# Optimization experiments

Hardware: AMD Instinct MI355X
Metric: run time of the kernel (lower is better)

Reference implementation:

```python
import jax, jax.numpy as jnp
import numpy as np

RADIUS = 0.8
NSAMPLE = 32
EPS = 1e-5  # BatchNorm eps


def _bn(x, gamma, beta, axes):
    # BatchNorm (training-mode batch statistics), channel dim kept via broadcasting
    m = jnp.mean(x, axis=axes, keepdims=True)
    v = jnp.var(x, axis=axes, keepdims=True)
    return (x - m) * jax.lax.rsqrt(v + EPS) * gamma + beta


def setup_inputs() -> dict:
    key = jax.random.key(0)
    ks = jax.random.split(key, 6)
    B, N, P, C, COUT = 4, 8192, 2048, 128, 256
    ffps_xyz = jax.random.uniform(ks[0], (B, P, 3), dtype=jnp.float32) * 2.0 - 1.0
    backbone_xyz = jax.random.uniform(ks[1], (B, N, 3), dtype=jnp.float32) * 2.0 - 1.0
    backbone_features = jax.random.normal(ks[2], (B, C, N), dtype=jnp.float32)
    w_shift = jax.random.normal(ks[3], (3, 3), dtype=jnp.float32) * 0.1
    gamma_shift = jnp.ones((3,), jnp.float32)
    beta_shift = jnp.zeros((3,), jnp.float32)
    w_mlp = jax.random.normal(ks[4], (COUT, 3 + C), dtype=jnp.float32) * 0.05
    gamma_mlp = jnp.ones((COUT,), jnp.float32)
    beta_mlp = jnp.zeros((COUT,), jnp.float32)
    return {
        "ffps_xyz": ffps_xyz,
        "backbone_xyz": backbone_xyz,
        "backbone_features": backbone_features,
        "w_shift": w_shift,
        "gamma_shift": gamma_shift,
        "beta_shift": beta_shift,
        "w_mlp": w_mlp,
        "gamma_mlp": gamma_mlp,
        "beta_mlp": beta_mlp,
    }


def reference(ffps_xyz, backbone_xyz, backbone_features,
              w_shift, gamma_shift, beta_shift,
              w_mlp, gamma_mlp, beta_mlp):
    B, P, _ = ffps_xyz.shape
    N = backbone_xyz.shape[1]

    # ---- shift_layer: Conv1d(3->3, k=1, no bias) + BN1d + ReLU on (B,3,P) ----
    x = jnp.einsum('oc,bpc->bop', w_shift, ffps_xyz)                  # (B,3,P)
    x = _bn(x, gamma_shift[None, :, None], beta_shift[None, :, None], (0, 2))
    new_xyz = jax.nn.relu(x).transpose(0, 2, 1)                       # (B,P,3) query centers

    # ---- QueryAndGroup: ball query (radius, nsample), use_xyz=True ----
    d2 = jnp.sum((new_xyz[:, :, None, :] - backbone_xyz[:, None, :, :]) ** 2, -1)  # (B,P,N)
    within = d2 < (RADIUS * RADIUS)
    # pick the first NSAMPLE in-radius indices (CUDA ball_query semantics)
    keyv = jnp.where(within, jnp.arange(N, dtype=jnp.int32), jnp.int32(N))
    negk, idx = jax.lax.top_k(-keyv, NSAMPLE)                          # smallest keys first
    valid = (-negk) < N
    idx = jnp.where(valid, idx, idx[..., :1])                          # pad with first found idx

    g_xyz = jnp.take_along_axis(backbone_xyz[:, None, :, :], idx[..., None], axis=2)
    g_xyz = g_xyz - new_xyz[:, :, None, :]                             # (B,P,S,3) recentered
    feats = backbone_features.transpose(0, 2, 1)                       # (B,N,C)
    g_f = jnp.take_along_axis(feats[:, None, :, :], idx[..., None], axis=2)  # (B,P,S,C)
    g = jnp.concatenate([g_xyz, g_f], axis=-1)                         # (B,P,S,3+C)

    # ---- mlp: 1x1 conv (3+C -> COUT, no bias) + BN + ReLU ----
    y = jnp.einsum('oc,bpsc->bops', w_mlp, g)                          # (B,COUT,P,S)
    y = _bn(y, gamma_mlp[None, :, None, None], beta_mlp[None, :, None, None], (0, 2, 3))
    y = jax.nn.relu(y)

    # ---- max-pool over neighbor axis, squeeze, transpose ----
    y = jnp.max(y, axis=3)                                             # (B,COUT,P)
    return y.transpose(0, 2, 1)                                        # (B,P,COUT)
```

## Files before the change

kernel.cpp:

```cpp
#include <hip/hip_runtime.h>
#include <math.h>

namespace {
constexpr int B    = 4;
constexpr int N    = 8192;
constexpr int P    = 2048;
constexpr int C    = 128;
constexpr int COUT = 256;
constexpr int NS   = 32;
constexpr int BP   = B * P;
constexpr int BPB  = 2;
constexpr int GRP  = 8;
constexpr int NBLK = BP / (BPB * GRP);

constexpr size_t OFF_FEATT = 0;
constexpr size_t OFF_WSWZ  = 8388608;
constexpr size_t OFF_NXD   = 8470528;
constexpr size_t OFF_NXF   = 8667136;
constexpr size_t OFF_IDX   = 8765440;
constexpr size_t OFF_YMAX  = 9814016;
constexpr size_t OFF_PART  = 18202624;
constexpr size_t OFF_P2    = 19251200;
constexpr size_t OFF_AB    = 19513344;
constexpr size_t WS_NEED   = 19515392;
}

typedef short bf16x8 __attribute__((ext_vector_type(8)));
typedef float f32x4  __attribute__((ext_vector_type(4)));

typedef const __attribute__((address_space(1))) void gas_void;
typedef __attribute__((address_space(3))) void las_void;
#define GLOBAL_LOAD_LDS16(gp, lp) \
    __builtin_amdgcn_global_load_lds((gas_void*)(gp), (las_void*)(lp), 16, 0, 0)

__device__ inline unsigned short f2bf(float f) {
    unsigned u = __float_as_uint(f);
    unsigned r = u + 0x7fffu + ((u >> 16) & 1u);
    return (unsigned short)(r >> 16);
}

__global__ __launch_bounds__(256) void k_transpose(const float* __restrict__ feat,
                                                   unsigned short* __restrict__ featT) {
    __shared__ float tile[64][33];
    int tx = threadIdx.x, ty = threadIdx.y;
    int n0 = blockIdx.x * 32, c0 = blockIdx.y * 64, b = blockIdx.z;
    const float* src = feat + ((size_t)b * C + c0) * N + n0;
#pragma unroll
    for (int j = 0; j < 8; j++) tile[ty + 8 * j][tx] = src[(size_t)(ty + 8 * j) * N + tx];
    __syncthreads();
    int t = ty * 32 + tx;
    int n = t >> 3;
    int k8 = (t & 7) * 8;
    unsigned vv[4];
#pragma unroll
    for (int i = 0; i < 4; i++) {
        unsigned lo = f2bf(tile[k8 + 2 * i][n]);
        unsigned hi = f2bf(tile[k8 + 2 * i + 1][n]);
        vv[i] = lo | (hi << 16);
    }
    *(int4*)&featT[((size_t)b * N + n0 + n) * C + c0 + k8] =
        make_int4((int)vv[0], (int)vv[1], (int)vv[2], (int)vv[3]);
}

__global__ __launch_bounds__(256) void k_wswz(const float* __restrict__ w,
                                              unsigned short* __restrict__ wswz) {
    int i = blockIdx.x * 256 + threadIdx.x;
    int j = i & 7;
    int lane = (i >> 3) & 63;
    int rest = i >> 9;
    int ks = rest % 5, rt = rest / 5;
    int cout = rt * 16 + (lane & 15);
    int k = ks * 32 + (lane >> 4) * 8 + j;
    float v = 0.f;
    if (k < 128) v = w[cout * 131 + 3 + k];
    else if (k < 131) v = w[cout * 131 + (k - 128)];
    wswz[i] = f2bf(v);
}

__global__ __launch_bounds__(1024) void k_shift(const float* __restrict__ ffps,
                                                const float* __restrict__ wsh,
                                                const float* __restrict__ gam,
                                                const float* __restrict__ bet,
                                                double* __restrict__ nxd,
                                                float* __restrict__ nxf) {
#pragma clang fp contract(off)
    __shared__ double red[6][1024];
    __shared__ double par[6];
    int t = threadIdx.x;
    double w[9];
#pragma unroll
    for (int i = 0; i < 9; i++) w[i] = (double)wsh[i];
    double x[8][3];
    double s[3] = {0, 0, 0}, sq[3] = {0, 0, 0};
#pragma unroll
    for (int i = 0; i < 8; i++) {
        int p = t + 1024 * i;
        double f0 = (double)ffps[p * 3 + 0];
        double f1 = (double)ffps[p * 3 + 1];
        double f2 = (double)ffps[p * 3 + 2];
#pragma unroll
        for (int o = 0; o < 3; o++) {
            double xo = (w[o * 3 + 0] * f0 + w[o * 3 + 1] * f1) + w[o * 3 + 2] * f2;
            x[i][o] = xo;
            s[o] += xo;
            sq[o] += xo * xo;
        }
    }
#pragma unroll
    for (int o = 0; o < 3; o++) { red[o][t] = s[o]; red[3 + o][t] = sq[o]; }
    for (int off = 512; off > 0; off >>= 1) {
        __syncthreads();
        if (t < off) {
#pragma unroll
            for (int j = 0; j < 6; j++) red[j][t] += red[j][t + off];
        }
    }
    __syncthreads();
    if (t == 0) {
#pragma unroll
        for (int o = 0; o < 3; o++) {
            double m = red[o][0] / (double)BP;
            double v = red[3 + o][0] / (double)BP - m * m;
            par[o] = m;
            par[3 + o] = 1.0 / sqrt(v + 1e-5);
        }
    }
    __syncthreads();
    double gv[3] = {(double)gam[0], (double)gam[1], (double)gam[2]};
    double bv[3] = {(double)bet[0], (double)bet[1], (double)bet[2]};
#pragma unroll
    for (int i = 0; i < 8; i++) {
        int p = t + 1024 * i;
#pragma unroll
        for (int o = 0; o < 3; o++) {
            double y = ((x[i][o] - par[o]) * par[3 + o]) * gv[o] + bv[o];
            y = (y > 0.0) ? y : 0.0;
            nxd[p * 3 + o] = y;
            nxf[p * 3 + o] = (float)y;
        }
    }
}

__global__ __launch_bounds__(256) void k_ballq(const float* __restrict__ bbxyz,
                                               const double* __restrict__ nxd,
                                               int* __restrict__ idxo) {
#pragma clang fp contract(off)
    int t = threadIdx.x;
    int wv = t >> 6, lane = t & 63;
    int q = blockIdx.x * 4 + wv;
    int b = q >> 11;
    double qx = nxd[q * 3 + 0], qy = nxd[q * 3 + 1], qz = nxd[q * 3 + 2];
    const double R2 = 0.8 * 0.8;
    {
        double ex = fmax(fmax(qx - 1.0, -1.0 - qx), 0.0);
        double ey = fmax(fmax(qy - 1.0, -1.0 - qy), 0.0);
        double ez = fmax(fmax(qz - 1.0, -1.0 - qz), 0.0);
        if (ex * ex + ey * ey + ez * ez >= R2) {
            if (lane < NS) idxo[q * NS + lane] = 0;
            return;
        }
    }
    const float* base = bbxyz + (size_t)b * N * 3;
    int found = 0, firstn = -1;

    float X0[8], Y0[8], Z0[8], X1[8], Y1[8], Z1[8], X2[8], Y2[8], Z2[8];

    auto loadb = [&](float (&XX)[8], float (&YY)[8], float (&ZZ)[8], int it) {
#pragma unroll
        for (int j = 0; j < 8; j++) {
            int n = it * 512 + j * 64 + lane;
            XX[j] = base[n * 3 + 0];
            YY[j] = base[n * 3 + 1];
            ZZ[j] = base[n * 3 + 2];
        }
    };
    auto proc = [&](float (&XX)[8], float (&YY)[8], float (&ZZ)[8], int it) {
#pragma clang fp contract(off)
#pragma unroll
        for (int j = 0; j < 8; j++) {
            int n = it * 512 + j * 64 + lane;
            double dx = qx - (double)XX[j];
            double dy = qy - (double)YY[j];
            double dz = qz - (double)ZZ[j];
            double d2 = (dx * dx + dy * dy) + dz * dz;
            bool within = d2 < R2;
            unsigned long long mask = __ballot(within);
            if (firstn < 0 && mask != 0ull) firstn = (n - lane) + (__ffsll(mask) - 1);
            if (within) {
                int rank = found + __popcll(mask & ((1ull << lane) - 1ull));
                if (rank < NS) idxo[q * NS + rank] = n;
            }
            found += __popcll(mask);
        }
    };

    loadb(X0, Y0, Z0, 0);
    loadb(X1, Y1, Z1, 1);
    loadb(X2, Y2, Z2, 2);

    for (int itb = 0; itb < 16; itb += 3) {
        proc(X0, Y0, Z0, itb);
        if (found >= NS) break;
        loadb(X0, Y0, Z0, (itb + 3 < 16) ? itb + 3 : 0);
        if (itb + 1 >= 16) break;
        proc(X1, Y1, Z1, itb + 1);
        if (found >= NS) break;
        loadb(X1, Y1, Z1, (itb + 4 < 16) ? itb + 4 : 0);
        if (itb + 2 >= 16) break;
        proc(X2, Y2, Z2, itb + 2);
        if (found >= NS) break;
        loadb(X2, Y2, Z2, (itb + 5 < 16) ? itb + 5 : 0);
    }
    if (found < NS) {
        int padv = (found == 0) ? 0 : firstn;
        if (lane >= found && lane < NS) idxo[q * NS + lane] = padv;
    }
}

__global__ __launch_bounds__(256, 2) void k_mlp_mfma(
        const float* __restrict__ bbxyz,
        const unsigned short* __restrict__ featT,
        const unsigned short* __restrict__ wswz,
        const float* __restrict__ nxf,
        const int* __restrict__ idx,
        float* __restrict__ ymax,
        float* __restrict__ partial) {
    __shared__ alignas(16) unsigned short G[2][4 * 4 * 64 * 8];
    int t = threadIdx.x, lane = t & 63, w = t >> 6;
    int q = lane >> 4, c16 = lane & 15;
    int blk = blockIdx.x;
    int bpbase = blk * (BPB * GRP);
    const bf16x8* wp = (const bf16x8*)wswz;

    bf16x8 wreg[5][4];
#pragma unroll
    for (int ks = 0; ks < 5; ks++)
#pragma unroll
        for (int nt = 0; nt < 4; nt++)
            wreg[ks][nt] = wp[((w * 4 + nt) * 5 + ks) * 64 + lane];

    int n_cur[4], n_nxt[4], n_nx2[4];
#pragma unroll
    for (int mt = 0; mt < 4; mt++)
        n_cur[mt] = idx[(bpbase + (mt >> 1)) * NS + (mt & 1) * 16 + c16];
#pragma unroll
    for (int mt = 0; mt < 4; mt++)
        n_nxt[mt] = idx[(bpbase + BPB + (mt >> 1)) * NS + (mt & 1) * 16 + c16];
    {
        int bp = bpbase + (w >> 1);
        const unsigned short* row = featT + ((size_t)(bp >> 11) * N + n_cur[w]) * C + q * 8;
#pragma unroll
        for (int ks = 0; ks < 4; ks++)
            GLOBAL_LOAD_LDS16(row + ks * 32, &G[0][(w * 4 + ks) * 512]);
    }

    float smA[4] = {0.f, 0.f, 0.f, 0.f}, sqA[4] = {0.f, 0.f, 0.f, 0.f};

    for (int g = 0; g < GRP; g++) {
        int buf = g & 1;
        int bp0 = bpbase + g * BPB;
        if (g + 2 < GRP) {
#pragma unroll
            for (int mt = 0; mt < 4; mt++)
                n_nx2[mt] = idx[(bp0 + 2 * BPB + (mt >> 1)) * NS + (mt & 1) * 16 + c16];
        }
        __syncthreads();
        if (g + 1 < GRP) {
            int bp = bp0 + BPB + (w >> 1);
            const unsigned short* row = featT + ((size_t)(bp >> 11) * N + n_nxt[w]) * C + q * 8;
#pragma unroll
            for (int ks = 0; ks < 4; ks++)
                GLOBAL_LOAD_LDS16(row + ks * 32, &G[buf ^ 1][(w * 4 + ks) * 512]);
        }

        f32x4 acc[4][4];
#pragma unroll
        for (int mt = 0; mt < 4; mt++)
#pragma unroll
            for (int nt = 0; nt < 4; nt++) acc[mt][nt] = (f32x4){0.f, 0.f, 0.f, 0.f};

#pragma unroll
        for (int ks = 0; ks < 4; ks++) {
            bf16x8 ag[4];
#pragma unroll
            for (int mt = 0; mt < 4; mt++)
                ag[mt] = *(const bf16x8*)&G[buf][((mt * 4 + ks) * 64 + lane) * 8];
#pragma unroll
            for (int nt = 0; nt < 4; nt++)
#pragma unroll
                for (int mt = 0; mt < 4; mt++)
                    acc[mt][nt] = __builtin_amdgcn_mfma_f32_16x16x32_bf16(ag[mt], wreg[ks][nt], acc[mt][nt], 0, 0, 0);
        }
        {
            bf16x8 agx[4];
#pragma unroll
            for (int mt = 0; mt < 4; mt++) {
                int bp = bp0 + (mt >> 1);
                unsigned u01 = 0, u23 = 0;
                if (q == 0) {
                    const float* src = bbxyz + ((size_t)(bp >> 11) * N + n_cur[mt]) * 3;
                    const float* ctr = nxf + bp * 3;
                    u01 = (unsigned)f2bf(src[0] - ctr[0]) | ((unsigned)f2bf(src[1] - ctr[1]) << 16);
                    u23 = (unsigned)f2bf(src[2] - ctr[2]);
                }
                union { int4 i; bf16x8 h; } u;
                u.i = make_int4((int)u01, (int)u23, 0, 0);
                agx[mt] = u.h;
            }
#pragma unroll
            for (int nt = 0; nt < 4; nt++)
#pragma unroll
                for (int mt = 0; mt < 4; mt++)
                    acc[mt][nt] = __builtin_amdgcn_mfma_f32_16x16x32_bf16(agx[mt], wreg[4][nt], acc[mt][nt], 0, 0, 0);
        }

#pragma unroll
        for (int pm = 0; pm < BPB; pm++) {
            int bp = bp0 + pm;
#pragma unroll
            for (int nt = 0; nt < 4; nt++) {
                f32x4 a = acc[2 * pm][nt], c = acc[2 * pm + 1][nt];
                float mx = fmaxf(fmaxf(fmaxf(a[0], a[1]), fmaxf(a[2], a[3])),
                                 fmaxf(fmaxf(c[0], c[1]), fmaxf(c[2], c[3])));
                smA[nt] += ((a[0] + a[1]) + (a[2] + a[3])) + ((c[0] + c[1]) + (c[2] + c[3]));
                sqA[nt] += ((a[0] * a[0] + a[1] * a[1]) + (a[2] * a[2] + a[3] * a[3])) +
                           ((c[0] * c[0] + c[1] * c[1]) + (c[2] * c[2] + c[3] * c[3]));
                mx = fmaxf(mx, __shfl_xor(mx, 16, 64));
                mx = fmaxf(mx, __shfl_xor(mx, 32, 64));
                if (q == 0)
                    ymax[(size_t)bp * COUT + w * 64 + nt * 16 + c16] = mx;
            }
        }
#pragma unroll
        for (int mt = 0; mt < 4; mt++) { n_cur[mt] = n_nxt[mt]; n_nxt[mt] = n_nx2[mt]; }
    }

#pragma unroll
    for (int nt = 0; nt < 4; nt++) {
        float sm = smA[nt], sq = sqA[nt];
        sm += __shfl_xor(sm, 16, 64);
        sm += __shfl_xor(sm, 32, 64);
        sq += __shfl_xor(sq, 16, 64);
        sq += __shfl_xor(sq, 32, 64);
        if (q == 0) {
            int cout = w * 64 + nt * 16 + c16;
            partial[(size_t)blk * 512 + cout] = sm;
            partial[(size_t)blk * 512 + 256 + cout] = sq;
        }
    }
}

__global__ __launch_bounds__(256) void k_red(const float* __restrict__ partial,
                                             float* __restrict__ p2) {
    int t = threadIdx.x, j = blockIdx.x;
    const float* row = partial + (size_t)j * 4 * 512;
    float s0 = 0.f, s1 = 0.f;
    for (int r = 0; r < 4; r++) {
        s0 += row[r * 512 + t];
        s1 += row[r * 512 + 256 + t];
    }
    p2[j * 512 + t] = s0;
    p2[j * 512 + 256 + t] = s1;
}

__global__ __launch_bounds__(256) void k_stats(const float* __restrict__ p2,
                                               const float* __restrict__ gam,
                                               const float* __restrict__ bet,
                                               float* __restrict__ ab) {
    int c = threadIdx.x;
    double sm = 0.0, sq = 0.0;
    for (int r = 0; r < 128; r++) {
        sm += (double)p2[r * 512 + c];
        sq += (double)p2[r * 512 + 256 + c];
    }
    const double cnt = (double)BP * (double)NS;
    double mean = sm / cnt;
    double var = sq / cnt - mean * mean;
    double a = (double)gam[c] / sqrt(var + 1e-5);
    double bb = (double)bet[c] - mean * a;
    ab[c] = (float)a;
    ab[256 + c] = (float)bb;
}

__global__ __launch_bounds__(256) void k_final(const float* __restrict__ ymax,
                                               const float* __restrict__ ab,
                                               float* __restrict__ out) {
    int i = blockIdx.x * 256 + threadIdx.x;
    int c0 = (i & 63) * 4;
    f32x4 y = *(const f32x4*)&ymax[(size_t)i * 4];
    f32x4 a = *(const f32x4*)&ab[c0];
    f32x4 bb = *(const f32x4*)&ab[256 + c0];
    f32x4 r;
#pragma unroll
    for (int j = 0; j < 4; j++) r[j] = fmaxf(a[j] * y[j] + bb[j], 0.f);
    *(f32x4*)&out[(size_t)i * 4] = r;
}

extern "C" void kernel_launch(void* const* d_in, const int* in_sizes, int n_in,
                              void* d_out, int out_size, void* d_ws, size_t ws_size,
                              hipStream_t stream) {
    const float* ffps  = (const float*)d_in[0];
    const float* bbxyz = (const float*)d_in[1];
    const float* feat  = (const float*)d_in[2];
    const float* wsh   = (const float*)d_in[3];
    const float* gsh   = (const float*)d_in[4];
    const float* bsh   = (const float*)d_in[5];
    const float* wml   = (const float*)d_in[6];
    const float* gml   = (const float*)d_in[7];
    const float* bml   = (const float*)d_in[8];
    float* out = (float*)d_out;
    char* ws = (char*)d_ws;
    if (ws_size < WS_NEED) return;

    unsigned short* featT = (unsigned short*)(ws + OFF_FEATT);
    unsigned short* wswz  = (unsigned short*)(ws + OFF_WSWZ);
    double*         nxd   = (double*)(ws + OFF_NXD);
    float*          nxf   = (float*)(ws + OFF_NXF);
    int*            idx   = (int*)(ws + OFF_IDX);
    float*          ymax  = (float*)(ws + OFF_YMAX);
    float*          part  = (float*)(ws + OFF_PART);
    float*          p2    = (float*)(ws + OFF_P2);
    float*          ab    = (float*)(ws + OFF_AB);

    k_transpose<<<dim3(N / 32, C / 64, B), dim3(32, 8, 1), 0, stream>>>(feat, featT);
    k_wswz<<<dim3(160), dim3(256), 0, stream>>>(wml, wswz);
    k_shift<<<dim3(1), dim3(1024), 0, stream>>>(ffps, wsh, gsh, bsh, nxd, nxf);
    k_ballq<<<dim3(BP / 4), dim3(256), 0, stream>>>(bbxyz, nxd, idx);
    k_mlp_mfma<<<dim3(NBLK), dim3(256), 0, stream>>>(bbxyz, featT, wswz, nxf, idx, ymax, part);
    k_red<<<dim3(128), dim3(256), 0, stream>>>(part, p2);
    k_stats<<<dim3(1), dim3(256), 0, stream>>>(p2, gml, bml, ab);
    k_final<<<dim3(BP * COUT / 1024), dim3(256), 0, stream>>>(ymax, ab, out);
}
```

Measured before the change: 169.9 us.

## Fuse front-end kernels and replace partial-sum reduction with atomics

Eight launches are collapsed into four. A multi-block prep kernel produces the shift-layer partial statistics, and one combined front kernel runs the feature transpose, weight swizzle, shift normalisation and ball query. The MLP kernel now accumulates the BN statistics with float atomics into zeroed sums, and the final kernel computes the scale and shift inline, so the separate reduction and stats kernels go away. This removes launch gaps and the serial single-block kernels, but float atomic accumulation makes the summation order nondeterministic, and every final block recomputes the per-channel statistics.

```diff
diff --git a/kernel.cpp b/kernel.cpp
--- a/kernel.cpp
+++ b/kernel.cpp
@@ -15,14 +15,12 @@
 
 constexpr size_t OFF_FEATT = 0;
 constexpr size_t OFF_WSWZ  = 8388608;
-constexpr size_t OFF_NXD   = 8470528;
-constexpr size_t OFF_NXF   = 8667136;
-constexpr size_t OFF_IDX   = 8765440;
-constexpr size_t OFF_YMAX  = 9814016;
-constexpr size_t OFF_PART  = 18202624;
-constexpr size_t OFF_P2    = 19251200;
-constexpr size_t OFF_AB    = 19513344;
-constexpr size_t WS_NEED   = 19515392;
+constexpr size_t OFF_SSLOT = 8470528;
+constexpr size_t OFF_SUMS  = 8471040;
+constexpr size_t OFF_NXF   = 8475136;
+constexpr size_t OFF_IDX   = 8573440;
+constexpr size_t OFF_YMAX  = 9622016;
+constexpr size_t WS_NEED   = 18010624;
 }
 
 typedef short bf16x8 __attribute__((ext_vector_type(8)));
@@ -39,76 +37,37 @@
     return (unsigned short)(r >> 16);
 }
 
-__global__ __launch_bounds__(256) void k_transpose(const float* __restrict__ feat,
-                                                   unsigned short* __restrict__ featT) {
-    __shared__ float tile[64][33];
-    int tx = threadIdx.x, ty = threadIdx.y;
-    int n0 = blockIdx.x * 32, c0 = blockIdx.y * 64, b = blockIdx.z;
-    const float* src = feat + ((size_t)b * C + c0) * N + n0;
-#pragma unroll
-    for (int j = 0; j < 8; j++) tile[ty + 8 * j][tx] = src[(size_t)(ty + 8 * j) * N + tx];
-    __syncthreads();
-    int t = ty * 32 + tx;
-    int n = t >> 3;
-    int k8 = (t & 7) * 8;
-    unsigned vv[4];
+__global__ __launch_bounds__(256) void k_prep(const float* __restrict__ ffps,
+                                              const float* __restrict__ wsh,
+                                              double* __restrict__ sslot,
+                                              float* __restrict__ sums) {
+#pragma clang fp contract(off)
+    int blk = blockIdx.x, t = threadIdx.x;
+    if (blk == 8) {
+        ((f32x4*)sums)[t & 127] = (f32x4){0.f, 0.f, 0.f, 0.f};
+        return;
+    }
+    __shared__ double red[6][256];
+    double w[9];
+#pragma unroll
+    for (int i = 0; i < 9; i++) w[i] = (double)wsh[i];
+    double s[3] = {0, 0, 0}, sq[3] = {0, 0, 0};
 #pragma unroll
     for (int i = 0; i < 4; i++) {
-        unsigned lo = f2bf(tile[k8 + 2 * i][n]);
-        unsigned hi = f2bf(tile[k8 + 2 * i + 1][n]);
-        vv[i] = lo | (hi << 16);
-    }
-    *(int4*)&featT[((size_t)b * N + n0 + n) * C + c0 + k8] =
-        make_int4((int)vv[0], (int)vv[1], (int)vv[2], (int)vv[3]);
-}
-
-__global__ __launch_bounds__(256) void k_wswz(const float* __restrict__ w,
-                                              unsigned short* __restrict__ wswz) {
-    int i = blockIdx.x * 256 + threadIdx.x;
-    int j = i & 7;
-    int lane = (i >> 3) & 63;
-    int rest = i >> 9;
-    int ks = rest % 5, rt = rest / 5;
-    int cout = rt * 16 + (lane & 15);
-    int k = ks * 32 + (lane >> 4) * 8 + j;
-    float v = 0.f;
-    if (k < 128) v = w[cout * 131 + 3 + k];
-    else if (k < 131) v = w[cout * 131 + (k - 128)];
-    wswz[i] = f2bf(v);
-}
-
-__global__ __launch_bounds__(1024) void k_shift(const float* __restrict__ ffps,
-                                                const float* __restrict__ wsh,
-                                                const float* __restrict__ gam,
-                                                const float* __restrict__ bet,
-                                                double* __restrict__ nxd,
-                                                float* __restrict__ nxf) {
-#pragma clang fp contract(off)
-    __shared__ double red[6][1024];
-    __shared__ double par[6];
-    int t = threadIdx.x;
-    double w[9];
-#pragma unroll
-    for (int i = 0; i < 9; i++) w[i] = (double)wsh[i];
-    double x[8][3];
-    double s[3] = {0, 0, 0}, sq[3] = {0, 0, 0};
-#pragma unroll
-    for (int i = 0; i < 8; i++) {
-        int p = t + 1024 * i;
+        int p = blk * 1024 + t + 256 * i;
         double f0 = (double)ffps[p * 3 + 0];
         double f1 = (double)ffps[p * 3 + 1];
         double f2 = (double)ffps[p * 3 + 2];
 #pragma unroll
         for (int o = 0; o < 3; o++) {
             double xo = (w[o * 3 + 0] * f0 + w[o * 3 + 1] * f1) + w[o * 3 + 2] * f2;
-            x[i][o] = xo;
             s[o] += xo;
             sq[o] += xo * xo;
         }
     }
 #pragma unroll
     for (int o = 0; o < 3; o++) { red[o][t] = s[o]; red[3 + o][t] = sq[o]; }
-    for (int off = 512; off > 0; off >>= 1) {
+    for (int off = 128; off > 0; off >>= 1) {
         __syncthreads();
         if (t < off) {
 #pragma unroll
@@ -116,40 +75,90 @@
         }
     }
     __syncthreads();
-    if (t == 0) {
-#pragma unroll
-        for (int o = 0; o < 3; o++) {
-            double m = red[o][0] / (double)BP;
-            double v = red[3 + o][0] / (double)BP - m * m;
-            par[o] = m;
-            par[3 + o] = 1.0 / sqrt(v + 1e-5);
-        }
-    }
-    __syncthreads();
-    double gv[3] = {(double)gam[0], (double)gam[1], (double)gam[2]};
-    double bv[3] = {(double)bet[0], (double)bet[1], (double)bet[2]};
-#pragma unroll
-    for (int i = 0; i < 8; i++) {
-        int p = t + 1024 * i;
-#pragma unroll
-        for (int o = 0; o < 3; o++) {
-            double y = ((x[i][o] - par[o]) * par[3 + o]) * gv[o] + bv[o];
-            y = (y > 0.0) ? y : 0.0;
-            nxd[p * 3 + o] = y;
-            nxf[p * 3 + o] = (float)y;
-        }
-    }
-}
-
-__global__ __launch_bounds__(256) void k_ballq(const float* __restrict__ bbxyz,
-                                               const double* __restrict__ nxd,
+    if (t < 6) sslot[blk * 6 + t] = red[t][0];
+}
+
+__global__ __launch_bounds__(256) void k_front(const float* __restrict__ ffps,
+                                               const float* __restrict__ bbxyz,
+                                               const float* __restrict__ feat,
+                                               const float* __restrict__ wsh,
+                                               const float* __restrict__ gsh,
+                                               const float* __restrict__ bsh,
+                                               const float* __restrict__ wml,
+                                               const double* __restrict__ sslot,
+                                               unsigned short* __restrict__ featT,
+                                               unsigned short* __restrict__ wswz,
+                                               float* __restrict__ nxf,
                                                int* __restrict__ idxo) {
 #pragma clang fp contract(off)
-    int t = threadIdx.x;
+    int blk = blockIdx.x, t = threadIdx.x;
+    if (blk >= 2048) {
+        int rb = blk - 2048;
+        if (rb < 2048) {
+            __shared__ float tile[64][33];
+            int tx = t & 31, ty = t >> 5;
+            int n0 = (rb & 255) * 32, c0 = ((rb >> 8) & 1) * 64, b = rb >> 9;
+            const float* src = feat + ((size_t)b * C + c0) * N + n0;
+#pragma unroll
+            for (int j = 0; j < 8; j++) tile[ty + 8 * j][tx] = src[(size_t)(ty + 8 * j) * N + tx];
+            __syncthreads();
+            int n = t >> 3;
+            int k8 = (t & 7) * 8;
+            unsigned vv[4];
+#pragma unroll
+            for (int i = 0; i < 4; i++) {
+                unsigned lo = f2bf(tile[k8 + 2 * i][n]);
+                unsigned hi = f2bf(tile[k8 + 2 * i + 1][n]);
+                vv[i] = lo | (hi << 16);
+            }
+            *(int4*)&featT[((size_t)b * N + n0 + n) * C + c0 + k8] =
+                make_int4((int)vv[0], (int)vv[1], (int)vv[2], (int)vv[3]);
+        } else {
+            int i = (rb - 2048) * 256 + t;
+            int j = i & 7;
+            int lane = (i >> 3) & 63;
+            int rest = i >> 9;
+            int ks = rest % 5, rt = rest / 5;
+            int cout = rt * 16 + (lane & 15);
+            int k = ks * 32 + (lane >> 4) * 8 + j;
+            float v = 0.f;
+            if (k < 128) v = wml[cout * 131 + 3 + k];
+            else if (k < 131) v = wml[cout * 131 + (k - 128)];
+            wswz[i] = f2bf(v);
+        }
+        return;
+    }
+
+    __shared__ double spar[6];
+    if (t < 6) {
+        double a = 0.0;
+        for (int r = 0; r < 8; r++) a += sslot[r * 6 + t];
+        spar[t] = a;
+    }
+    __syncthreads();
     int wv = t >> 6, lane = t & 63;
-    int q = blockIdx.x * 4 + wv;
+    int q = blk * 4 + wv;
     int b = q >> 11;
-    double qx = nxd[q * 3 + 0], qy = nxd[q * 3 + 1], qz = nxd[q * 3 + 2];
+    double f0 = (double)ffps[q * 3 + 0];
+    double f1 = (double)ffps[q * 3 + 1];
+    double f2 = (double)ffps[q * 3 + 2];
+    double qd[3];
+#pragma unroll
+    for (int o = 0; o < 3; o++) {
+        double m  = spar[o] * (1.0 / 8192.0);
+        double v  = spar[3 + o] * (1.0 / 8192.0) - m * m;
+        double is = 1.0 / sqrt(v + 1e-5);
+        double x  = ((double)wsh[o * 3 + 0] * f0 + (double)wsh[o * 3 + 1] * f1) +
+                    (double)wsh[o * 3 + 2] * f2;
+        double y  = ((x - m) * is) * (double)gsh[o] + (double)bsh[o];
+        qd[o] = (y > 0.0) ? y : 0.0;
+    }
+    double qx = qd[0], qy = qd[1], qz = qd[2];
+    if (lane == 0) {
+        nxf[q * 3 + 0] = (float)qx;
+        nxf[q * 3 + 1] = (float)qy;
+        nxf[q * 3 + 2] = (float)qz;
+    }
     const double R2 = 0.8 * 0.8;
     {
         double ex = fmax(fmax(qx - 1.0, -1.0 - qx), 0.0);
@@ -224,7 +233,7 @@
         const float* __restrict__ nxf,
         const int* __restrict__ idx,
         float* __restrict__ ymax,
-        float* __restrict__ partial) {
+        float* __restrict__ sums) {
     __shared__ alignas(16) unsigned short G[2][4 * 4 * 64 * 8];
     int t = threadIdx.x, lane = t & 63, w = t >> 6;
     int q = lane >> 4, c16 = lane & 15;
@@ -344,55 +353,34 @@
         sq += __shfl_xor(sq, 32, 64);
         if (q == 0) {
             int cout = w * 64 + nt * 16 + c16;
-            partial[(size_t)blk * 512 + cout] = sm;
-            partial[(size_t)blk * 512 + 256 + cout] = sq;
-        }
-    }
-}
-
-__global__ __launch_bounds__(256) void k_red(const float* __restrict__ partial,
-                                             float* __restrict__ p2) {
-    int t = threadIdx.x, j = blockIdx.x;
-    const float* row = partial + (size_t)j * 4 * 512;
-    float s0 = 0.f, s1 = 0.f;
-    for (int r = 0; r < 4; r++) {
-        s0 += row[r * 512 + t];
-        s1 += row[r * 512 + 256 + t];
-    }
-    p2[j * 512 + t] = s0;
-    p2[j * 512 + 256 + t] = s1;
-}
-
-__global__ __launch_bounds__(256) void k_stats(const float* __restrict__ p2,
+            atomicAdd(&sums[cout], sm);
+            atomicAdd(&sums[256 + cout], sq);
+        }
+    }
+}
+
+__global__ __launch_bounds__(256) void k_final(const float* __restrict__ ymax,
+                                               const float* __restrict__ sums,
                                                const float* __restrict__ gam,
                                                const float* __restrict__ bet,
-                                               float* __restrict__ ab) {
-    int c = threadIdx.x;
-    double sm = 0.0, sq = 0.0;
-    for (int r = 0; r < 128; r++) {
-        sm += (double)p2[r * 512 + c];
-        sq += (double)p2[r * 512 + 256 + c];
-    }
-    const double cnt = (double)BP * (double)NS;
-    double mean = sm / cnt;
-    double var = sq / cnt - mean * mean;
-    double a = (double)gam[c] / sqrt(var + 1e-5);
-    double bb = (double)bet[c] - mean * a;
-    ab[c] = (float)a;
-    ab[256 + c] = (float)bb;
-}
-
-__global__ __launch_bounds__(256) void k_final(const float* __restrict__ ymax,
-                                               const float* __restrict__ ab,
                                                float* __restrict__ out) {
-    int i = blockIdx.x * 256 + threadIdx.x;
-    int c0 = (i & 63) * 4;
+    __shared__ float sa[256], sb[256];
+    int t = threadIdx.x;
+    {
+        double sm = (double)sums[t], sq = (double)sums[256 + t];
+        double mean = sm * (1.0 / 262144.0);
+        double var = sq * (1.0 / 262144.0) - mean * mean;
+        double a = (double)gam[t] / sqrt(var + 1e-5);
+        sa[t] = (float)a;
+        sb[t] = (float)((double)bet[t] - mean * a);
+    }
+    __syncthreads();
+    int i = blockIdx.x * 256 + t;
+    int c0 = (t & 63) * 4;
     f32x4 y = *(const f32x4*)&ymax[(size_t)i * 4];
-    f32x4 a = *(const f32x4*)&ab[c0];
-    f32x4 bb = *(const f32x4*)&ab[256 + c0];
     f32x4 r;
 #pragma unroll
-    for (int j = 0; j < 4; j++) r[j] = fmaxf(a[j] * y[j] + bb[j], 0.f);
+    for (int j = 0; j < 4; j++) r[j] = fmaxf(sa[c0 + j] * y[j] + sb[c0 + j], 0.f);
     *(f32x4*)&out[(size_t)i * 4] = r;
 }
 
@@ -414,20 +402,15 @@
 
     unsigned short* featT = (unsigned short*)(ws + OFF_FEATT);
     unsigned short* wswz  = (unsigned short*)(ws + OFF_WSWZ);
-    double*         nxd   = (double*)(ws + OFF_NXD);
+    double*         sslot = (double*)(ws + OFF_SSLOT);
+    float*          sums  = (float*)(ws + OFF_SUMS);
     float*          nxf   = (float*)(ws + OFF_NXF);
     int*            idx   = (int*)(ws + OFF_IDX);
     float*          ymax  = (float*)(ws + OFF_YMAX);
-    float*          part  = (float*)(ws + OFF_PART);
-    float*          p2    = (float*)(ws + OFF_P2);
-    float*          ab    = (float*)(ws + OFF_AB);
-
-    k_transpose<<<dim3(N / 32, C / 64, B), dim3(32, 8, 1), 0, stream>>>(feat, featT);
-    k_wswz<<<dim3(160), dim3(256), 0, stream>>>(wml, wswz);
-    k_shift<<<dim3(1), dim3(1024), 0, stream>>>(ffps, wsh, gsh, bsh, nxd, nxf);
-    k_ballq<<<dim3(BP / 4), dim3(256), 0, stream>>>(bbxyz, nxd, idx);
-    k_mlp_mfma<<<dim3(NBLK), dim3(256), 0, stream>>>(bbxyz, featT, wswz, nxf, idx, ymax, part);
-    k_red<<<dim3(128), dim3(256), 0, stream>>>(part, p2);
-    k_stats<<<dim3(1), dim3(256), 0, stream>>>(p2, gml, bml, ab);
-    k_final<<<dim3(BP * COUT / 1024), dim3(256), 0, stream>>>(ymax, ab, out);
-}
+
+    k_prep<<<dim3(9), dim3(256), 0, stream>>>(ffps, wsh, sslot, sums);
+    k_front<<<dim3(2048 + 2048 + 160), dim3(256), 0, stream>>>(
+        ffps, bbxyz, feat, wsh, gsh, bsh, wml, sslot, featT, wswz, nxf, idx);
+    k_mlp_mfma<<<dim3(NBLK), dim3(256), 0, stream>>>(bbxyz, featT, wswz, nxf, idx, ymax, sums);
+    k_final<<<dim3(BP * COUT / 1024), dim3(256), 0, stream>>>(ymax, sums, gml, bml, out);
+}
```

New measurement: 158.3 us. -6.8%, faster.
